# Kernel tuning notes

Measured on AMD Instinct MI355X. Metric: run time of the kernel, lower is better.

## Reference

```python
import jax, jax.numpy as jnp
import numpy as np

DIM = 1024
HEADS = 8
DIM_HEAD = 64
INNER = HEADS * DIM_HEAD  # 512
SCALE = 8.0


def l2norm(t, eps=1e-12):
    # matches F.normalize(t, dim=-1)
    n = jnp.linalg.norm(t, axis=-1, keepdims=True)
    return t / jnp.maximum(n, eps)


def setup_inputs() -> dict:
    key = jax.random.key(0)
    ks = jax.random.split(key, 5)
    x = jax.random.normal(ks[0], (4, 2048, DIM), dtype=jnp.float32)
    # torch Linear weights are [out, in]; store transposed [in, out] for x @ W
    s = 1.0 / np.sqrt(DIM)
    Wq = jax.random.uniform(ks[1], (DIM, INNER), jnp.float32, -s, s)
    Wk = jax.random.uniform(ks[2], (DIM, INNER), jnp.float32, -s, s)
    Wv = jax.random.uniform(ks[3], (DIM, INNER), jnp.float32, -s, s)
    so = 1.0 / np.sqrt(INNER)
    Wo = jax.random.uniform(ks[4], (INNER, DIM), jnp.float32, -so, so)
    return {"x": x, "Wq": Wq, "Wk": Wk, "Wv": Wv, "Wo": Wo}


def reference(x, Wq, Wk, Wv, Wo):
    b, n, _ = x.shape
    def split_heads(t):
        return t.reshape(b, n, HEADS, DIM_HEAD).transpose(0, 2, 1, 3)  # b h n d
    q = split_heads(x @ Wq)
    k = split_heads(x @ Wk)
    v = split_heads(x @ Wv)
    # cosine-sim attention: l2-normalize q, k then fixed scale
    q = l2norm(q)
    k = l2norm(k)
    sim = jnp.einsum('bhid,bhjd->bhij', q, k) * SCALE
    causal_mask = jnp.triu(jnp.ones((n, n), dtype=bool), k=1)
    sim = jnp.where(causal_mask, jnp.finfo(sim.dtype).min, sim)
    attn = jax.nn.softmax(sim, axis=-1)
    o = jnp.einsum('bhij,bhjd->bhid', attn, v)
    o = o.transpose(0, 2, 1, 3).reshape(b, n, INNER)
    return o @ Wo
```

## Files before the change

### kernel.cpp

```cpp
#include <hip/hip_runtime.h>
#include <hip/hip_bf16.h>

typedef __attribute__((ext_vector_type(8))) __bf16 bf16x8;
typedef __attribute__((ext_vector_type(4))) __bf16 bf16x4;
typedef __attribute__((ext_vector_type(4))) float f32x4;

#define MFMA16(a, b, c) __builtin_amdgcn_mfma_f32_16x16x32_bf16(a, b, c, 0, 0, 0)

static __device__ __forceinline__ ushort f2b(float f) {
    __bf16 b = (__bf16)f;
    return __builtin_bit_cast(ushort, b);
}
static __device__ __forceinline__ bf16x8 cat44(bf16x4 a, bf16x4 b) {
    bf16x8 r;
    r[0] = a[0]; r[1] = a[1]; r[2] = a[2]; r[3] = a[3];
    r[4] = b[0]; r[5] = b[1]; r[6] = b[2]; r[7] = b[3];
    return r;
}
static __device__ __forceinline__ void gload_lds16(const ushort* g, ushort* l) {
    __builtin_amdgcn_global_load_lds(
        (const __attribute__((address_space(1))) unsigned int*)g,
        (__attribute__((address_space(3))) unsigned int*)l, 16, 0, 0);
}

__global__ void f32_to_bf16_k(const float* __restrict__ in, ushort* __restrict__ out, int n4) {
    int i = blockIdx.x * blockDim.x + threadIdx.x;
    if (i >= n4) return;
    float4 v = reinterpret_cast<const float4*>(in)[i];
    ushort4 o;
    o.x = f2b(v.x); o.y = f2b(v.y); o.z = f2b(v.z); o.w = f2b(v.w);
    reinterpret_cast<ushort4*>(out)[i] = o;
}

__global__ __launch_bounds__(256)
void transpose_all_k(const float* __restrict__ Wq, const float* __restrict__ Wk,
                     const float* __restrict__ Wv, const float* __restrict__ Wo,
                     ushort* __restrict__ Wqkv, ushort* __restrict__ Wot) {
    __shared__ ushort T[64][72];
    const int bid = blockIdx.x;
    const int job = bid >> 7;
    const int t = bid & 127;
    const float* src; ushort* dst; int K, N;
    if (job == 0)      { src = Wq; dst = Wqkv;                      K = 1024; N = 512; }
    else if (job == 1) { src = Wk; dst = Wqkv + (size_t)512 * 1024; K = 1024; N = 512; }
    else if (job == 2) { src = Wv; dst = Wqkv + (size_t)1024 * 1024; K = 1024; N = 512; }
    else               { src = Wo; dst = Wot;                       K = 512;  N = 1024; }
    const int tn = N >> 6;
    const int bk = t / tn, bn = t - bk * tn;
    const int k0 = bk * 64, n0 = bn * 64;
    const int tid = threadIdx.x;
#pragma unroll
    for (int q = 0; q < 4; ++q) {
        const int lin = tid + 256 * q;
        const int kr = lin >> 4;
        const int n4 = (lin & 15) << 2;
        float4 v = *reinterpret_cast<const float4*>(&src[(size_t)(k0 + kr) * N + n0 + n4]);
        T[n4 + 0][kr] = f2b(v.x);
        T[n4 + 1][kr] = f2b(v.y);
        T[n4 + 2][kr] = f2b(v.z);
        T[n4 + 3][kr] = f2b(v.w);
    }
    __syncthreads();
#pragma unroll
    for (int s = 0; s < 2; ++s) {
        const int lin = tid + 256 * s;
        const int n = lin >> 3;
        const int kc = (lin & 7) << 3;
        ushort4 a, b;
        a.x = T[n][kc + 0]; a.y = T[n][kc + 1]; a.z = T[n][kc + 2]; a.w = T[n][kc + 3];
        b.x = T[n][kc + 4]; b.y = T[n][kc + 5]; b.z = T[n][kc + 6]; b.w = T[n][kc + 7];
        ushort* p = &dst[(size_t)(n0 + n) * K + k0 + kc];
        *reinterpret_cast<ushort4*>(p) = a;
        *reinterpret_cast<ushort4*>(p + 4) = b;
    }
}

template <int F32OUT, int ROUTE>
__global__ __launch_bounds__(256)
void gemm_tile_k(const ushort* __restrict__ A, const ushort* __restrict__ Bt,
                 void* __restrict__ C0, void* __restrict__ C1, void* __restrict__ C2,
                 int M, int N, int K, int nby) {
    __shared__ __align__(16) ushort As[128 * 32];
    __shared__ __align__(16) ushort Bs[128 * 32];
    const int tid = threadIdx.x;
    const int lane = tid & 63;
    const int w = tid >> 6;
    const int l15 = lane & 15, g = lane >> 4;
    const int wr = w >> 1, wc = w & 1;

    const int nwg = gridDim.x;
    const int cpx = nwg >> 3;
    const int bid = blockIdx.x;
    const int swz = (bid & 7) * cpx + (bid >> 3);
    const int bx = swz / nby, by = swz - bx * nby;
    const int rbase = bx * 128, cbase = by * 128;

    const int srow = lane >> 2;
    const int scol = (lane & 3) * 8;
    const ushort* Aw0 = A + (size_t)(rbase + 32 * w + srow) * K + scol;
    const ushort* Bw0 = Bt + (size_t)(cbase + 32 * w + srow) * K + scol;

    f32x4 acc[4][4];
#pragma unroll
    for (int m = 0; m < 4; ++m)
#pragma unroll
        for (int n = 0; n < 4; ++n) acc[m][n] = (f32x4){0, 0, 0, 0};

    const int nk = K >> 5;
    for (int kt = 0; kt < nk; ++kt) {
        const int k0 = kt << 5;
        if (kt) __syncthreads();
        gload_lds16(Aw0 + k0,          &As[(32 * w) * 32]);
        gload_lds16(Aw0 + 16 * K + k0, &As[(32 * w + 16) * 32]);
        gload_lds16(Bw0 + k0,          &Bs[(32 * w) * 32]);
        gload_lds16(Bw0 + 16 * K + k0, &Bs[(32 * w + 16) * 32]);
        __syncthreads();
        bf16x8 af[4], bf[4];
#pragma unroll
        for (int m = 0; m < 4; ++m)
            af[m] = *reinterpret_cast<const bf16x8*>(&As[(64 * wr + 16 * m + l15) * 32 + 8 * g]);
#pragma unroll
        for (int n = 0; n < 4; ++n)
            bf[n] = *reinterpret_cast<const bf16x8*>(&Bs[(64 * wc + 16 * n + l15) * 32 + 8 * g]);
#pragma unroll
        for (int m = 0; m < 4; ++m)
#pragma unroll
            for (int n = 0; n < 4; ++n)
                acc[m][n] = MFMA16(af[m], bf[n], acc[m][n]);
    }

    if (ROUTE) {
        const int col0 = cbase + 64 * wc;
        const int grp = col0 >> 9;
        const int co0 = col0 & 511;
        if (grp == 2) {
            const int h = co0 >> 6;
#pragma unroll
            for (int m = 0; m < 4; ++m) {
                const int row = rbase + 64 * wr + 16 * m + 4 * g;
                const int bb = row >> 11;
                const int tok = row & 2047;
#pragma unroll
                for (int n = 0; n < 4; ++n) {
                    const int d = 16 * n + l15;
                    bf16x4 wv;
#pragma unroll
                    for (int r = 0; r < 4; ++r) wv[r] = (__bf16)acc[m][n][r];
                    ushort* dst = (ushort*)C2 + (((size_t)(bb * 8 + h) * 64 + d) * 2048 + tok);
                    *reinterpret_cast<bf16x4*>(dst) = wv;
                }
            }
        } else {
            ushort* Cg = (ushort*)(grp == 0 ? C0 : C1);
#pragma unroll
            for (int m = 0; m < 4; ++m) {
                f32x4 ss = {0, 0, 0, 0};
#pragma unroll
                for (int n = 0; n < 4; ++n)
#pragma unroll
                    for (int r = 0; r < 4; ++r) ss[r] += acc[m][n][r] * acc[m][n][r];
#pragma unroll
                for (int r = 0; r < 4; ++r) {
                    float s = ss[r];
                    s += __shfl_xor(s, 1);
                    s += __shfl_xor(s, 2);
                    s += __shfl_xor(s, 4);
                    s += __shfl_xor(s, 8);
                    ss[r] = 1.0f / fmaxf(sqrtf(s), 1e-12f);
                }
                const int row = rbase + 64 * wr + 16 * m + 4 * g;
#pragma unroll
                for (int n = 0; n < 4; ++n) {
                    const int co = co0 + 16 * n + l15;
#pragma unroll
                    for (int r = 0; r < 4; ++r)
                        Cg[(size_t)(row + r) * 512 + co] = f2b(acc[m][n][r] * ss[r]);
                }
            }
        }
    } else {
#pragma unroll
        for (int m = 0; m < 4; ++m)
#pragma unroll
            for (int n = 0; n < 4; ++n) {
                const int row = rbase + 64 * wr + 16 * m + 4 * g;
                const int col = cbase + 64 * wc + 16 * n + l15;
                if (F32OUT) {
#pragma unroll
                    for (int r = 0; r < 4; ++r)
                        reinterpret_cast<float*>(C0)[(size_t)(row + r) * N + col] = acc[m][n][r];
                } else {
#pragma unroll
                    for (int r = 0; r < 4; ++r)
                        reinterpret_cast<ushort*>(C0)[(size_t)(row + r) * N + col] = f2b(acc[m][n][r]);
                }
            }
    }
}

__global__ __launch_bounds__(128, 2)
void flash_attn_k(const ushort* __restrict__ Q, const ushort* __restrict__ K,
                  const ushort* __restrict__ Vt, ushort* __restrict__ O) {
    __shared__ __align__(16) ushort Ks[64 * 64];
    __shared__ __align__(16) ushort Vs[64 * 64];
    const int tid = threadIdx.x;
    const int lane = tid & 63;
    const int wave = tid >> 6;
    const int l15 = lane & 15;
    const int g = lane >> 4;
    const int bh = blockIdx.x;
    const int b = bh >> 3, h = bh & 7;
    const int j = blockIdx.y;
    const int ytrue = (j < 16) ? j : 47 - j;
    const int wglob = ytrue * 2 + wave;
    const int c0 = wglob;
    const int c1 = 127 - wglob;
    const int q0 = c0 * 16 + l15;
    const int q1 = c1 * 16 + l15;
    const int nt0 = (c0 * 16 + 79) >> 6;
    const int nt1 = (c1 * 16 + 79) >> 6;
    const int ntb = ((127 - 2 * ytrue) * 16 + 79) >> 6;

    const ushort* Qb = Q + (size_t)(b * 2048) * 512 + h * 64;
    const ushort* Kb = K + (size_t)(b * 2048) * 512 + h * 64;
    const ushort* Vb = Vt + (size_t)bh * 64 * 2048;

    const ushort* kSrc[4];
    const ushort* vSrc[4];
    ushort* kDst[4];
    ushort* vDst[4];
#pragma unroll
    for (int i = 0; i < 4; ++i) {
        const int s = tid + 128 * i;
        const int row = s >> 3;
        const int cc = s & 7;
        const int sc = cc ^ (row & 7);
        kSrc[i] = Kb + (size_t)row * 512 + sc * 8;
        vSrc[i] = Vb + (size_t)row * 2048 + sc * 8;
        const int base = (wave * 64 + 128 * i) * 8;
        kDst[i] = &Ks[base];
        vDst[i] = &Vs[base];
    }

    bf16x8 qf0[2], qf1[2];
#pragma unroll
    for (int kh = 0; kh < 2; ++kh) {
        qf0[kh] = *reinterpret_cast<const bf16x8*>(Qb + (size_t)q0 * 512 + 32 * kh + 8 * g);
        qf1[kh] = *reinterpret_cast<const bf16x8*>(Qb + (size_t)q1 * 512 + 32 * kh + 8 * g);
    }

    f32x4 acc0[4], acc1[4];
#pragma unroll
    for (int d = 0; d < 4; ++d) {
        acc0[d] = (f32x4){0, 0, 0, 0};
        acc1[d] = (f32x4){0, 0, 0, 0};
    }
    float ls0 = 0.0f, ls1 = 0.0f;

    for (int t = 0; t < ntb; ++t) {
        if (t) __syncthreads();
#pragma unroll
        for (int i = 0; i < 4; ++i) gload_lds16(kSrc[i] + (size_t)t * 32768, kDst[i]);
#pragma unroll
        for (int i = 0; i < 4; ++i) gload_lds16(vSrc[i] + t * 64, vDst[i]);
        __syncthreads();

        if (t >= nt1) continue;
        const bool act0 = (t < nt0);
        const bool mk0 = (t == nt0 - 1);
        const bool mk1 = (t == nt1 - 1);

        bf16x8 af[4][2];
#pragma unroll
        for (int jt = 0; jt < 4; ++jt)
#pragma unroll
            for (int kh = 0; kh < 2; ++kh) {
                const int row = jt * 16 + l15;
                const int chunk = (g + 4 * kh) ^ (row & 7);
                af[jt][kh] = *reinterpret_cast<const bf16x8*>(&Ks[row * 64 + chunk * 8]);
            }
        bf16x4 vf[4][2][2];
#pragma unroll
        for (int d = 0; d < 4; ++d)
#pragma unroll
            for (int kk = 0; kk < 2; ++kk)
#pragma unroll
                for (int th = 0; th < 2; ++th) {
                    const int dr = d * 16 + l15;
                    const int chunk = ((g >> 1) + 2 * th + 4 * kk) ^ (dr & 7);
                    vf[d][kk][th] = *reinterpret_cast<const bf16x4*>(
                        &Vs[dr * 64 + chunk * 8 + (g & 1) * 4]);
                }

        f32x4 s1[4];
#pragma unroll
        for (int jt = 0; jt < 4; ++jt) {
            f32x4 z = {0, 0, 0, 0};
            z = MFMA16(af[jt][0], qf1[0], z);
            s1[jt] = MFMA16(af[jt][1], qf1[1], z);
        }

        bf16x8 pt1[2];
        float la1 = 0.0f;
#pragma unroll
        for (int jt = 0; jt < 4; ++jt) {
#pragma unroll
            for (int r = 0; r < 4; ++r) {
                float p = __expf(fmaf(s1[jt][r], 8.0f, -8.0f));
                if (mk1) {
                    int jj = t * 64 + jt * 16 + 4 * g + r;
                    p = (jj <= q1) ? p : 0.0f;
                }
                la1 += p;
                pt1[jt >> 1][(jt & 1) * 4 + r] = (__bf16)p;
            }
        }
        ls1 += la1;

#pragma unroll
        for (int d = 0; d < 4; ++d) {
            bf16x8 v0 = cat44(vf[d][0][0], vf[d][0][1]);
            bf16x8 v1 = cat44(vf[d][1][0], vf[d][1][1]);
            acc1[d] = MFMA16(v0, pt1[0], acc1[d]);
            acc1[d] = MFMA16(v1, pt1[1], acc1[d]);
        }

        if (act0) {
            f32x4 s0[4];
#pragma unroll
            for (int jt = 0; jt < 4; ++jt) {
                f32x4 z = {0, 0, 0, 0};
                z = MFMA16(af[jt][0], qf0[0], z);
                s0[jt] = MFMA16(af[jt][1], qf0[1], z);
            }
            bf16x8 pt0[2];
            float la0 = 0.0f;
#pragma unroll
            for (int jt = 0; jt < 4; ++jt) {
#pragma unroll
                for (int r = 0; r < 4; ++r) {
                    float p = __expf(fmaf(s0[jt][r], 8.0f, -8.0f));
                    if (mk0) {
                        int jj = t * 64 + jt * 16 + 4 * g + r;
                        p = (jj <= q0) ? p : 0.0f;
                    }
                    la0 += p;
                    pt0[jt >> 1][(jt & 1) * 4 + r] = (__bf16)p;
                }
            }
            ls0 += la0;
#pragma unroll
            for (int d = 0; d < 4; ++d) {
                bf16x8 v0 = cat44(vf[d][0][0], vf[d][0][1]);
                bf16x8 v1 = cat44(vf[d][1][0], vf[d][1][1]);
                acc0[d] = MFMA16(v0, pt0[0], acc0[d]);
                acc0[d] = MFMA16(v1, pt0[1], acc0[d]);
            }
        }
    }

    auto fin = [&](f32x4 (&acc)[4], float ls, int qr) {
        ls += __shfl_xor(ls, 16);
        ls += __shfl_xor(ls, 32);
        float inv = 1.0f / ls;
        ushort* Ob = O + (size_t)(b * 2048 + qr) * 512 + h * 64;
#pragma unroll
        for (int d = 0; d < 4; ++d) {
            bf16x4 w;
#pragma unroll
            for (int r = 0; r < 4; ++r) w[r] = (__bf16)(acc[d][r] * inv);
            *reinterpret_cast<bf16x4*>(Ob + d * 16 + 4 * g) = w;
        }
    };
    fin(acc1, ls1, q1);
    fin(acc0, ls0, q0);
}

extern "C" void kernel_launch(void* const* d_in, const int* in_sizes, int n_in,
                              void* d_out, int out_size, void* d_ws, size_t ws_size,
                              hipStream_t stream) {
    const float* x  = (const float*)d_in[0];
    const float* Wq = (const float*)d_in[1];
    const float* Wk = (const float*)d_in[2];
    const float* Wv = (const float*)d_in[3];
    const float* Wo = (const float*)d_in[4];
    float* out = (float*)d_out;

    char* ws = (char*)d_ws;
    ushort* xb  = (ushort*)ws; ws += (size_t)8192 * 1024 * 2;
    ushort* Wqt = (ushort*)ws; ws += (size_t)1536 * 1024 * 2;
    ushort* Wot = (ushort*)ws; ws += (size_t)1024 * 512 * 2;
    ushort* Qm  = (ushort*)ws; ws += (size_t)8192 * 512 * 2;
    ushort* Km  = (ushort*)ws; ws += (size_t)8192 * 512 * 2;
    ushort* Vtm = (ushort*)ws; ws += (size_t)8192 * 512 * 2;
    ushort* Om  = xb;

    f32_to_bf16_k<<<8192, 256, 0, stream>>>(x, xb, 2097152);
    transpose_all_k<<<512, 256, 0, stream>>>(Wq, Wk, Wv, Wo, Wqt, Wot);

    gemm_tile_k<0, 1><<<768, 256, 0, stream>>>(xb, Wqt, Qm, Km, Vtm, 8192, 1536, 1024, 12);

    flash_attn_k<<<dim3(32, 32), 128, 0, stream>>>(Qm, Km, Vtm, Om);

    gemm_tile_k<1, 0><<<512, 256, 0, stream>>>(Om, Wot, out, nullptr, nullptr, 8192, 1024, 512, 8);
}
```

Baseline: 108.3 us.

## Double-buffer LDS tiles in GEMM and flash attention to overlap loads

Both the GEMM and the flash-attention kernels now hold two LDS buffers for their K-tiles. The next tile is prefetched with global_load_lds right after the barrier, while the current tile is being computed, which leaves one barrier per iteration instead of two. The goal is to hide global-memory latency behind the MFMA work. The cost is double the LDS footprint in both kernels. Also, if the compiler inserts a conservative vmcnt wait before the LDS reads, the loads may not actually overlap with compute.

```diff
diff --git a/kernel.cpp b/kernel.cpp
--- a/kernel.cpp
+++ b/kernel.cpp
@@ -80,8 +80,8 @@
 void gemm_tile_k(const ushort* __restrict__ A, const ushort* __restrict__ Bt,
                  void* __restrict__ C0, void* __restrict__ C1, void* __restrict__ C2,
                  int M, int N, int K, int nby) {
-    __shared__ __align__(16) ushort As[128 * 32];
-    __shared__ __align__(16) ushort Bs[128 * 32];
+    __shared__ __align__(16) ushort As[2][128 * 32];
+    __shared__ __align__(16) ushort Bs[2][128 * 32];
     const int tid = threadIdx.x;
     const int lane = tid & 63;
     const int w = tid >> 6;
@@ -100,6 +100,14 @@
     const ushort* Aw0 = A + (size_t)(rbase + 32 * w + srow) * K + scol;
     const ushort* Bw0 = Bt + (size_t)(cbase + 32 * w + srow) * K + scol;
 
+    auto stage = [&](int kt, int buf) {
+        const int k0 = kt << 5;
+        gload_lds16(Aw0 + k0,          &As[buf][(32 * w) * 32]);
+        gload_lds16(Aw0 + 16 * K + k0, &As[buf][(32 * w + 16) * 32]);
+        gload_lds16(Bw0 + k0,          &Bs[buf][(32 * w) * 32]);
+        gload_lds16(Bw0 + 16 * K + k0, &Bs[buf][(32 * w + 16) * 32]);
+    };
+
     f32x4 acc[4][4];
 #pragma unroll
     for (int m = 0; m < 4; ++m)
@@ -107,21 +115,19 @@
         for (int n = 0; n < 4; ++n) acc[m][n] = (f32x4){0, 0, 0, 0};
 
     const int nk = K >> 5;
+    stage(0, 0);
     for (int kt = 0; kt < nk; ++kt) {
-        const int k0 = kt << 5;
-        if (kt) __syncthreads();
-        gload_lds16(Aw0 + k0,          &As[(32 * w) * 32]);
-        gload_lds16(Aw0 + 16 * K + k0, &As[(32 * w + 16) * 32]);
-        gload_lds16(Bw0 + k0,          &Bs[(32 * w) * 32]);
-        gload_lds16(Bw0 + 16 * K + k0, &Bs[(32 * w + 16) * 32]);
         __syncthreads();
+        if (kt + 1 < nk) stage(kt + 1, (kt + 1) & 1);
+        const ushort* Asb = As[kt & 1];
+        const ushort* Bsb = Bs[kt & 1];
         bf16x8 af[4], bf[4];
 #pragma unroll
         for (int m = 0; m < 4; ++m)
-            af[m] = *reinterpret_cast<const bf16x8*>(&As[(64 * wr + 16 * m + l15) * 32 + 8 * g]);
+            af[m] = *reinterpret_cast<const bf16x8*>(&Asb[(64 * wr + 16 * m + l15) * 32 + 8 * g]);
 #pragma unroll
         for (int n = 0; n < 4; ++n)
-            bf[n] = *reinterpret_cast<const bf16x8*>(&Bs[(64 * wc + 16 * n + l15) * 32 + 8 * g]);
+            bf[n] = *reinterpret_cast<const bf16x8*>(&Bsb[(64 * wc + 16 * n + l15) * 32 + 8 * g]);
 #pragma unroll
         for (int m = 0; m < 4; ++m)
 #pragma unroll
@@ -201,8 +207,8 @@
 __global__ __launch_bounds__(128, 2)
 void flash_attn_k(const ushort* __restrict__ Q, const ushort* __restrict__ K,
                   const ushort* __restrict__ Vt, ushort* __restrict__ O) {
-    __shared__ __align__(16) ushort Ks[64 * 64];
-    __shared__ __align__(16) ushort Vs[64 * 64];
+    __shared__ __align__(16) ushort Ks[2][64 * 64];
+    __shared__ __align__(16) ushort Vs[2][64 * 64];
     const int tid = threadIdx.x;
     const int lane = tid & 63;
     const int wave = tid >> 6;
@@ -227,8 +233,7 @@
 
     const ushort* kSrc[4];
     const ushort* vSrc[4];
-    ushort* kDst[4];
-    ushort* vDst[4];
+    int dOff[4];
 #pragma unroll
     for (int i = 0; i < 4; ++i) {
         const int s = tid + 128 * i;
@@ -237,10 +242,15 @@
         const int sc = cc ^ (row & 7);
         kSrc[i] = Kb + (size_t)row * 512 + sc * 8;
         vSrc[i] = Vb + (size_t)row * 2048 + sc * 8;
-        const int base = (wave * 64 + 128 * i) * 8;
-        kDst[i] = &Ks[base];
-        vDst[i] = &Vs[base];
-    }
+        dOff[i] = (wave * 64 + 128 * i) * 8;
+    }
+
+    auto stage = [&](int t, int buf) {
+#pragma unroll
+        for (int i = 0; i < 4; ++i) gload_lds16(kSrc[i] + (size_t)t * 32768, &Ks[buf][dOff[i]]);
+#pragma unroll
+        for (int i = 0; i < 4; ++i) gload_lds16(vSrc[i] + t * 64, &Vs[buf][dOff[i]]);
+    };
 
     bf16x8 qf0[2], qf1[2];
 #pragma unroll
@@ -257,15 +267,13 @@
     }
     float ls0 = 0.0f, ls1 = 0.0f;
 
+    stage(0, 0);
     for (int t = 0; t < ntb; ++t) {
-        if (t) __syncthreads();
-#pragma unroll
-        for (int i = 0; i < 4; ++i) gload_lds16(kSrc[i] + (size_t)t * 32768, kDst[i]);
-#pragma unroll
-        for (int i = 0; i < 4; ++i) gload_lds16(vSrc[i] + t * 64, vDst[i]);
         __syncthreads();
-
+        if (t + 1 < ntb) stage(t + 1, (t + 1) & 1);
         if (t >= nt1) continue;
+        const ushort* Kbf = Ks[t & 1];
+        const ushort* Vbf = Vs[t & 1];
         const bool act0 = (t < nt0);
         const bool mk0 = (t == nt0 - 1);
         const bool mk1 = (t == nt1 - 1);
@@ -277,7 +285,7 @@
             for (int kh = 0; kh < 2; ++kh) {
                 const int row = jt * 16 + l15;
                 const int chunk = (g + 4 * kh) ^ (row & 7);
-                af[jt][kh] = *reinterpret_cast<const bf16x8*>(&Ks[row * 64 + chunk * 8]);
+                af[jt][kh] = *reinterpret_cast<const bf16x8*>(&Kbf[row * 64 + chunk * 8]);
             }
         bf16x4 vf[4][2][2];
 #pragma unroll
@@ -289,7 +297,7 @@
                     const int dr = d * 16 + l15;
                     const int chunk = ((g >> 1) + 2 * th + 4 * kk) ^ (dr & 7);
                     vf[d][kk][th] = *reinterpret_cast<const bf16x4*>(
-                        &Vs[dr * 64 + chunk * 8 + (g & 1) * 4]);
+                        &Vbf[dr * 64 + chunk * 8 + (g & 1) * 4]);
                 }
 
         f32x4 s1[4];
```

Result: no change. 110.4 us (+1.9%).

## Use raw exp2, MFMA row-sums, hoisted QK for both tiles, and setprio

Applied to the files above, without the earlier changes.

Replaces __expf(8s-8) with a direct v_exp_f32 on the argument prescaled by 8*log2(e). The softmax denominator is now computed with an MFMA against a ones vector, so the per-element scalar additions and the final cross-lane shuffles are no longer needed. Both query tiles' QK MFMAs are issued up front, and s_setprio brackets the PV MFMAs to improve interleaving across waves. The risks are higher register pressure and reliance on MFMA accumulator layout for the sum, which also uses the bf16-rounded probabilities.

```diff
diff --git a/kernel.cpp b/kernel.cpp
--- a/kernel.cpp
+++ b/kernel.cpp
@@ -21,6 +21,11 @@
     __builtin_amdgcn_global_load_lds(
         (const __attribute__((address_space(1))) unsigned int*)g,
         (__attribute__((address_space(3))) unsigned int*)l, 16, 0, 0);
+}
+static __device__ __forceinline__ float exp2_fast(float x) {
+    float r;
+    asm("v_exp_f32 %0, %1" : "=v"(r) : "v"(x));
+    return r;
 }
 
 __global__ void f32_to_bf16_k(const float* __restrict__ in, ushort* __restrict__ out, int n4) {
@@ -221,6 +226,8 @@
     const int nt1 = (c1 * 16 + 79) >> 6;
     const int ntb = ((127 - 2 * ytrue) * 16 + 79) >> 6;
 
+    const float CEXP = 11.5415603f;
+
     const ushort* Qb = Q + (size_t)(b * 2048) * 512 + h * 64;
     const ushort* Kb = K + (size_t)(b * 2048) * 512 + h * 64;
     const ushort* Vb = Vt + (size_t)bh * 64 * 2048;
@@ -249,13 +256,17 @@
         qf1[kh] = *reinterpret_cast<const bf16x8*>(Qb + (size_t)q1 * 512 + 32 * kh + 8 * g);
     }
 
+    bf16x8 ones;
+#pragma unroll
+    for (int i = 0; i < 8; ++i) ones[i] = (__bf16)1.0f;
+
     f32x4 acc0[4], acc1[4];
 #pragma unroll
     for (int d = 0; d < 4; ++d) {
         acc0[d] = (f32x4){0, 0, 0, 0};
         acc1[d] = (f32x4){0, 0, 0, 0};
     }
-    float ls0 = 0.0f, ls1 = 0.0f;
+    f32x4 lac0 = {0, 0, 0, 0}, lac1 = {0, 0, 0, 0};
 
     for (int t = 0; t < ntb; ++t) {
         if (t) __syncthreads();
@@ -292,31 +303,37 @@
                         &Vs[dr * 64 + chunk * 8 + (g & 1) * 4]);
                 }
 
-        f32x4 s1[4];
+        f32x4 s1[4], s0[4];
 #pragma unroll
         for (int jt = 0; jt < 4; ++jt) {
             f32x4 z = {0, 0, 0, 0};
             z = MFMA16(af[jt][0], qf1[0], z);
             s1[jt] = MFMA16(af[jt][1], qf1[1], z);
         }
+        if (act0) {
+#pragma unroll
+            for (int jt = 0; jt < 4; ++jt) {
+                f32x4 z = {0, 0, 0, 0};
+                z = MFMA16(af[jt][0], qf0[0], z);
+                s0[jt] = MFMA16(af[jt][1], qf0[1], z);
+            }
+        }
 
         bf16x8 pt1[2];
-        float la1 = 0.0f;
 #pragma unroll
         for (int jt = 0; jt < 4; ++jt) {
 #pragma unroll
             for (int r = 0; r < 4; ++r) {
-                float p = __expf(fmaf(s1[jt][r], 8.0f, -8.0f));
+                float p = exp2_fast(fmaf(s1[jt][r], CEXP, -CEXP));
                 if (mk1) {
                     int jj = t * 64 + jt * 16 + 4 * g + r;
                     p = (jj <= q1) ? p : 0.0f;
                 }
-                la1 += p;
                 pt1[jt >> 1][(jt & 1) * 4 + r] = (__bf16)p;
             }
         }
-        ls1 += la1;
-
+
+        __builtin_amdgcn_s_setprio(1);
 #pragma unroll
         for (int d = 0; d < 4; ++d) {
             bf16x8 v0 = cat44(vf[d][0][0], vf[d][0][1]);
@@ -324,31 +341,25 @@
             acc1[d] = MFMA16(v0, pt1[0], acc1[d]);
             acc1[d] = MFMA16(v1, pt1[1], acc1[d]);
         }
+        lac1 = MFMA16(ones, pt1[0], lac1);
+        lac1 = MFMA16(ones, pt1[1], lac1);
+        __builtin_amdgcn_s_setprio(0);
 
         if (act0) {
-            f32x4 s0[4];
+            bf16x8 pt0[2];
 #pragma unroll
             for (int jt = 0; jt < 4; ++jt) {
-                f32x4 z = {0, 0, 0, 0};
-                z = MFMA16(af[jt][0], qf0[0], z);
-                s0[jt] = MFMA16(af[jt][1], qf0[1], z);
-            }
-            bf16x8 pt0[2];
-            float la0 = 0.0f;
-#pragma unroll
-            for (int jt = 0; jt < 4; ++jt) {
 #pragma unroll
                 for (int r = 0; r < 4; ++r) {
-                    float p = __expf(fmaf(s0[jt][r], 8.0f, -8.0f));
+                    float p = exp2_fast(fmaf(s0[jt][r], CEXP, -CEXP));
                     if (mk0) {
                         int jj = t * 64 + jt * 16 + 4 * g + r;
                         p = (jj <= q0) ? p : 0.0f;
                     }
-                    la0 += p;
                     pt0[jt >> 1][(jt & 1) * 4 + r] = (__bf16)p;
                 }
             }
-            ls0 += la0;
+            __builtin_amdgcn_s_setprio(1);
 #pragma unroll
             for (int d = 0; d < 4; ++d) {
                 bf16x8 v0 = cat44(vf[d][0][0], vf[d][0][1]);
@@ -356,12 +367,13 @@
                 acc0[d] = MFMA16(v0, pt0[0], acc0[d]);
                 acc0[d] = MFMA16(v1, pt0[1], acc0[d]);
             }
+            lac0 = MFMA16(ones, pt0[0], lac0);
+            lac0 = MFMA16(ones, pt0[1], lac0);
+            __builtin_amdgcn_s_setprio(0);
         }
     }
 
     auto fin = [&](f32x4 (&acc)[4], float ls, int qr) {
-        ls += __shfl_xor(ls, 16);
-        ls += __shfl_xor(ls, 32);
         float inv = 1.0f / ls;
         ushort* Ob = O + (size_t)(b * 2048 + qr) * 512 + h * 64;
 #pragma unroll
@@ -372,8 +384,8 @@
             *reinterpret_cast<bf16x4*>(Ob + d * 16 + 4 * g) = w;
         }
     };
-    fin(acc1, ls1, q1);
-    fin(acc0, ls0, q0);
+    fin(acc1, lac1[0], q1);
+    fin(acc0, lac0[0], q0);
 }
 
 extern "C" void kernel_launch(void* const* d_in, const int* in_sizes, int n_in,
```

Result: no change. 109.1 us (+0.8%).
